# Performance work log

Hardware: AMD Instinct MI355X
Metric: run time of the kernel (lower is better)

Reference implementation:

```python
import jax, jax.numpy as jnp
import numpy as np

B, S, D = 4, 2048, 1024
EPS = 1e-5


def setup_inputs() -> dict:
    key = jax.random.key(0)
    ks = jax.random.split(key, 8)
    s = 1.0 / np.sqrt(D)
    return {
        "x": jax.random.normal(ks[0], (B, S, D), dtype=jnp.float32),
        "Wq": jax.random.normal(ks[1], (D, D), dtype=jnp.float32) * s,
        "Wk": jax.random.normal(ks[2], (D, D), dtype=jnp.float32) * s,
        "Wv": jax.random.normal(ks[3], (D, D), dtype=jnp.float32) * s,
        "W1": jax.random.normal(ks[4], (D, D), dtype=jnp.float32) * s,
        "b1": jnp.zeros((D,), dtype=jnp.float32),
        "W2": jax.random.normal(ks[5], (D, D), dtype=jnp.float32) * s,
        "b2": jnp.zeros((D,), dtype=jnp.float32),
        "gamma": jnp.ones((D,), dtype=jnp.float32),
        "beta": jnp.zeros((D,), dtype=jnp.float32),
    }


def _layer_norm(x, gamma, beta):
    mu = jnp.mean(x, axis=-1, keepdims=True)
    var = jnp.mean(jnp.square(x - mu), axis=-1, keepdims=True)
    return (x - mu) * jax.lax.rsqrt(var + EPS) * gamma + beta


def reference(x, Wq, Wk, Wv, W1, b1, W2, b2, gamma, beta):
    seq_len, d = x.shape[1], x.shape[2]
    # torch Linear: y = x @ W.T
    Q = jnp.einsum('bsd,ed->bse', x, Wq)
    K = jnp.einsum('bsd,ed->bse', x, Wk)
    V = jnp.einsum('bsd,ed,->bse', x, Wv, jnp.float32(1.0)) if False else jnp.einsum('bsd,ed->bse', x, Wv)
    scores = jnp.einsum('bqd,bkd->bqk', Q, K) / jnp.sqrt(jnp.float32(d))
    causal = jnp.tril(jnp.ones((seq_len, seq_len), dtype=bool))  # [S,S]
    scores = jnp.where(causal[None, :, :], scores, -jnp.inf)
    attn = jax.nn.softmax(scores, axis=-1)
    attn_out = jnp.einsum('bqk,bkd->bqd', attn, V)
    # dropout is identity at eval
    h = _layer_norm(x + attn_out, gamma, beta)
    ff = jnp.einsum('bsd,ed->bse', jax.nn.relu(jnp.einsum('bsd,ed->bse', h, W1) + b1), W2) + b2
    out = _layer_norm(h + ff, gamma, beta)
    return out
```

## Files before the change

kernel.cpp:

```cpp
#include <hip/hip_runtime.h>
#include <math.h>
#include <cstdint>
#include <cstddef>

#define DI __device__ __forceinline__

typedef __bf16 bf16x8 __attribute__((ext_vector_type(8)));
typedef float f32x4 __attribute__((ext_vector_type(4)));

static constexpr int kB = 4, kS = 2048, kD = 1024;
static constexpr int kM = kB * kS;
static constexpr float kScale = 0.03125f;
static constexpr float kEps = 1e-5f;

DI unsigned short f2bf(float f) {
  unsigned u = __float_as_uint(f);
  u += 0x7FFFu + ((u >> 16) & 1u);
  return (unsigned short)(u >> 16);
}
DI float bf2f(unsigned short h) {
  return __uint_as_float(((unsigned)h) << 16);
}

DI void gld_lds16(const void* g, void* l) {
  __builtin_amdgcn_global_load_lds(
      (__attribute__((address_space(1))) void*)(void*)g,
      (__attribute__((address_space(3))) void*)l, 16, 0, 0);
}

__global__ __launch_bounds__(256) void k_cast_all(
    const float* __restrict__ x, const float* __restrict__ Wq,
    const float* __restrict__ Wk, const float* __restrict__ Wv,
    const float* __restrict__ W1, const float* __restrict__ W2,
    unsigned short* __restrict__ xb, unsigned short* __restrict__ Wqkb,
    unsigned short* __restrict__ Wvb, unsigned short* __restrict__ W1b,
    unsigned short* __restrict__ W2b) {
  const int i = blockIdx.x * 256 + threadIdx.x;
  const int X4 = kM * kD / 4;
  const int W4 = kD * kD / 4;
  const float* src;
  unsigned short* dst;
  int j;
  if (i < X4) { src = x; dst = xb; j = i; }
  else if (i < X4 + W4)     { src = Wq; dst = Wqkb;          j = i - X4; }
  else if (i < X4 + 2 * W4) { src = Wk; dst = Wqkb + 4 * W4; j = i - X4 - W4; }
  else if (i < X4 + 3 * W4) { src = Wv; dst = Wvb;           j = i - X4 - 2 * W4; }
  else if (i < X4 + 4 * W4) { src = W1; dst = W1b;           j = i - X4 - 3 * W4; }
  else                      { src = W2; dst = W2b;           j = i - X4 - 4 * W4; }
  float4 v = ((const float4*)src)[j];
  ushort4 o;
  o.x = f2bf(v.x); o.y = f2bf(v.y); o.z = f2bf(v.z); o.w = f2bf(v.w);
  ((ushort4*)dst)[j] = o;
}

template <int OUT_BF16, int RELU, int CAUSAL>
__global__ __launch_bounds__(256, 2) void k_gemm_nt(
    const unsigned short* __restrict__ A, const unsigned short* __restrict__ B,
    void* __restrict__ Cv, const float* __restrict__ bias,
    int M, int N, int K, int lda, int ldb, int ldc,
    long sA, long sB, long sC) {
  int bm, bn;
  {
    int lin = blockIdx.x + gridDim.x * blockIdx.y;
    const int nblk = gridDim.x * gridDim.y;
    if ((nblk & 7) == 0)
      lin = (lin & 7) * (nblk >> 3) + (lin >> 3);
    if (CAUSAL == 1) {
      const int t = lin;
      int r = (int)floorf((sqrtf(8.f * (float)t + 1.f) - 1.f) * 0.5f);
      while ((r + 1) * (r + 2) / 2 <= t) ++r;
      while (r * (r + 1) / 2 > t) --r;
      bm = r * 128;
      bn = (t - r * (r + 1) / 2) * 128;
    } else {
      bm = (lin / gridDim.x) * 128;
      bn = (lin % gridDim.x) * 128;
    }
  }
  A += (long)blockIdx.z * sA;
  B += (long)blockIdx.z * sB;

  const int tid = threadIdx.x;
  const int lane = tid & 63;
  const int wm = ((tid >> 6) >> 1) * 64;
  const int wn = ((tid >> 6) & 1) * 64;

  __shared__ __align__(16) unsigned short Asm[128 * 64];
  __shared__ __align__(16) unsigned short Bsm[128 * 64];

  f32x4 acc[4][4];
#pragma unroll
  for (int i = 0; i < 4; ++i)
#pragma unroll
    for (int j = 0; j < 4; ++j) acc[i][j] = (f32x4){0.f, 0.f, 0.f, 0.f};

  const int r_row = tid >> 3;
  const int dst_k = (tid & 7) * 8;
  const int src_k = ((tid & 7) ^ ((tid >> 3) & 7)) * 8;
  const int fm = lane & 15;
  const int fq = lane >> 4;

  for (int k0 = 0; k0 < K; k0 += 64) {
#pragma unroll
    for (int i = 0; i < 4; ++i) {
      const int row = i * 32 + r_row;
      gld_lds16(A + (long)(bm + row) * lda + (k0 + src_k), Asm + row * 64 + dst_k);
      gld_lds16(B + (long)(bn + row) * ldb + (k0 + src_k), Bsm + row * 64 + dst_k);
    }
    __syncthreads();
#pragma unroll
    for (int kk = 0; kk < 2; ++kk) {
      bf16x8 af[4], bfr[4];
#pragma unroll
      for (int i = 0; i < 4; ++i) {
        const int pa = ((kk * 4 + fq) ^ (fm & 7)) * 8;
        af[i]  = *(const bf16x8*)(Asm + (wm + i * 16 + fm) * 64 + pa);
        bfr[i] = *(const bf16x8*)(Bsm + (wn + i * 16 + fm) * 64 + pa);
      }
#pragma unroll
      for (int i = 0; i < 4; ++i)
#pragma unroll
        for (int j = 0; j < 4; ++j)
          acc[i][j] = __builtin_amdgcn_mfma_f32_16x16x32_bf16(af[i], bfr[j], acc[i][j], 0, 0, 0);
    }
    __syncthreads();
  }

  const long cb = (long)blockIdx.z * sC;
#pragma unroll
  for (int i = 0; i < 4; ++i) {
#pragma unroll
    for (int j = 0; j < 4; ++j) {
      const int col = bn + wn + j * 16 + fm;
      const float bv = bias ? bias[col] : 0.f;
#pragma unroll
      for (int r = 0; r < 4; ++r) {
        const int row = bm + wm + i * 16 + fq * 4 + r;
        float v = acc[i][j][r] + bv;
        if (RELU) v = fmaxf(v, 0.f);
        if (OUT_BF16)
          ((unsigned short*)Cv)[cb + (long)row * ldc + col] = f2bf(v);
        else
          ((float*)Cv)[cb + (long)row * ldc + col] = v;
      }
    }
  }
}

__global__ __launch_bounds__(256, 2) void k_attn_pv(
    const unsigned short* __restrict__ P, const unsigned short* __restrict__ Vt,
    unsigned short* __restrict__ O) {
  const int r = blockIdx.x;
  const int q = blockIdx.y + 16 * blockIdx.z;
  const int lx = q & 7;
  const int pq = r + 8 * (q >> 3);
  const int pair = pq & 15;
  const int zz = pq >> 4;

  const int bn = lx * 128;
  const int bm_hi = (31 - pair) * 64;
  const int bm_lo = pair * 64;
  const int Khi = bm_hi + 64;
  const int Klo = bm_lo + 64;
  P  += (long)zz * kS * kS;
  Vt += (long)zz * kD * kS;
  O  += (long)zz * kS * kD;

  const int tid = threadIdx.x;
  const int lane = tid & 63;
  const int wn = (tid >> 6) * 32;

  __shared__ __align__(16) unsigned short Ah[64 * 64];
  __shared__ __align__(16) unsigned short Al[64 * 64];
  __shared__ __align__(16) unsigned short Bs[128 * 64];

  f32x4 ah[4][2], al[4][2];
#pragma unroll
  for (int i = 0; i < 4; ++i)
#pragma unroll
    for (int j = 0; j < 2; ++j) {
      ah[i][j] = (f32x4){0.f, 0.f, 0.f, 0.f};
      al[i][j] = (f32x4){0.f, 0.f, 0.f, 0.f};
    }

  const int r_row = tid >> 3;
  const int dst_k = (tid & 7) * 8;
  const int src_k = ((tid & 7) ^ ((tid >> 3) & 7)) * 8;
  const int fm = lane & 15;
  const int fq = lane >> 4;

  for (int k0 = 0; k0 < Khi; k0 += 64) {
    const bool lo = (k0 < Klo);
#pragma unroll
    for (int i = 0; i < 2; ++i) {
      const int row = i * 32 + r_row;
      gld_lds16(P + (long)(bm_hi + row) * kS + (k0 + src_k), Ah + row * 64 + dst_k);
      if (lo)
        gld_lds16(P + (long)(bm_lo + row) * kS + (k0 + src_k), Al + row * 64 + dst_k);
    }
#pragma unroll
    for (int i = 0; i < 4; ++i) {
      const int row = i * 32 + r_row;
      gld_lds16(Vt + (long)(bn + row) * kS + (k0 + src_k), Bs + row * 64 + dst_k);
    }
    __syncthreads();
#pragma unroll
    for (int kk = 0; kk < 2; ++kk) {
      bf16x8 afh[4], afl[4], bfr[2];
#pragma unroll
      for (int i = 0; i < 4; ++i) {
        const int ra = i * 16 + fm;
        const int pa = ((kk * 4 + fq) ^ (ra & 7)) * 8;
        afh[i] = *(const bf16x8*)(Ah + ra * 64 + pa);
        afl[i] = *(const bf16x8*)(Al + ra * 64 + pa);
      }
#pragma unroll
      for (int j = 0; j < 2; ++j) {
        const int rb = wn + j * 16 + fm;
        const int pb = ((kk * 4 + fq) ^ (rb & 7)) * 8;
        bfr[j] = *(const bf16x8*)(Bs + rb * 64 + pb);
      }
#pragma unroll
      for (int i = 0; i < 4; ++i)
#pragma unroll
        for (int j = 0; j < 2; ++j)
          ah[i][j] = __builtin_amdgcn_mfma_f32_16x16x32_bf16(afh[i], bfr[j], ah[i][j], 0, 0, 0);
      if (lo) {
#pragma unroll
        for (int i = 0; i < 4; ++i)
#pragma unroll
          for (int j = 0; j < 2; ++j)
            al[i][j] = __builtin_amdgcn_mfma_f32_16x16x32_bf16(afl[i], bfr[j], al[i][j], 0, 0, 0);
      }
    }
    __syncthreads();
  }

#pragma unroll
  for (int i = 0; i < 4; ++i) {
#pragma unroll
    for (int j = 0; j < 2; ++j) {
      const int col = bn + wn + j * 16 + fm;
#pragma unroll
      for (int r2 = 0; r2 < 4; ++r2) {
        const int rr = i * 16 + fq * 4 + r2;
        O[(long)(bm_hi + rr) * kD + col] = f2bf(ah[i][j][r2]);
        O[(long)(bm_lo + rr) * kD + col] = f2bf(al[i][j][r2]);
      }
    }
  }
}

DI float wsum(float v) {
  v += __shfl_xor(v, 32, 64);
  v += __shfl_xor(v, 16, 64);
  v += __shfl_xor(v, 8, 64);
  v += __shfl_xor(v, 4, 64);
  v += __shfl_xor(v, 2, 64);
  v += __shfl_xor(v, 1, 64);
  return v;
}
DI float wmax(float v) {
  v = fmaxf(v, __shfl_xor(v, 32, 64));
  v = fmaxf(v, __shfl_xor(v, 16, 64));
  v = fmaxf(v, __shfl_xor(v, 8, 64));
  v = fmaxf(v, __shfl_xor(v, 4, 64));
  v = fmaxf(v, __shfl_xor(v, 2, 64));
  v = fmaxf(v, __shfl_xor(v, 1, 64));
  return v;
}

__global__ __launch_bounds__(256) void k_softmax_causal(
    const unsigned short* __restrict__ S, unsigned short* __restrict__ P) {
  const int row = blockIdx.x;
  const int q = row & (kS - 1);
  const int lim = (q & ~127) + 128;
  const unsigned short* Srow = S + (long)row * kS;
  unsigned short* Prow = P + (long)row * kS;
  const int tid = threadIdx.x;
  __shared__ float red[4];

  float v[8];
  float mx = -INFINITY;
#pragma unroll
  for (int i = 0; i < 8; ++i) {
    const int k = tid + i * 256;
    float xv = -INFINITY;
    if (k <= q) xv = bf2f(Srow[k]) * kScale;
    v[i] = xv;
    mx = fmaxf(mx, xv);
  }
  mx = wmax(mx);
  if ((tid & 63) == 0) red[tid >> 6] = mx;
  __syncthreads();
  mx = fmaxf(fmaxf(red[0], red[1]), fmaxf(red[2], red[3]));
  __syncthreads();

  float sum = 0.f;
#pragma unroll
  for (int i = 0; i < 8; ++i) {
    const float e = (v[i] > -INFINITY) ? __expf(v[i] - mx) : 0.f;
    v[i] = e;
    sum += e;
  }
  sum = wsum(sum);
  if ((tid & 63) == 0) red[tid >> 6] = sum;
  __syncthreads();
  sum = red[0] + red[1] + red[2] + red[3];
  const float inv = 1.f / sum;
#pragma unroll
  for (int i = 0; i < 8; ++i) {
    const int k = tid + i * 256;
    if (k < lim) Prow[k] = f2bf(v[i] * inv);
  }
}

template <int X_BF16, int OUT_FP32>
__global__ __launch_bounds__(256) void k_residual_ln(
    const void* __restrict__ Xv, const unsigned short* __restrict__ Yb,
    const float* __restrict__ gamma, const float* __restrict__ beta,
    float* __restrict__ Out, unsigned short* __restrict__ OutB) {
  const long base = (long)blockIdx.x * kD;
  const int tid = threadIdx.x;
  __shared__ float reds[4], redss[4];
  float v[4];
  float s = 0.f, ss2 = 0.f;
#pragma unroll
  for (int i = 0; i < 4; ++i) {
    const int k = tid + i * 256;
    const float xf = X_BF16 ? bf2f(((const unsigned short*)Xv)[base + k])
                            : ((const float*)Xv)[base + k];
    const float xv = xf + bf2f(Yb[base + k]);
    v[i] = xv;
    s += xv;
    ss2 += xv * xv;
  }
  s = wsum(s);
  ss2 = wsum(ss2);
  if ((tid & 63) == 0) { reds[tid >> 6] = s; redss[tid >> 6] = ss2; }
  __syncthreads();
  s = reds[0] + reds[1] + reds[2] + reds[3];
  ss2 = redss[0] + redss[1] + redss[2] + redss[3];
  const float mu = s * (1.f / kD);
  float var = ss2 * (1.f / kD) - mu * mu;
  var = fmaxf(var, 0.f);
  const float rstd = rsqrtf(var + kEps);
#pragma unroll
  for (int i = 0; i < 4; ++i) {
    const int k = tid + i * 256;
    const float y = (v[i] - mu) * rstd * gamma[k] + beta[k];
    if (OUT_FP32) Out[base + k] = y;
    else          OutB[base + k] = f2bf(y);
  }
}

extern "C" void kernel_launch(void* const* d_in, const int* in_sizes, int n_in,
                              void* d_out, int out_size, void* d_ws, size_t ws_size,
                              hipStream_t stream) {
  (void)in_sizes; (void)n_in; (void)out_size; (void)ws_size;
  const float* x     = (const float*)d_in[0];
  const float* Wq    = (const float*)d_in[1];
  const float* Wk    = (const float*)d_in[2];
  const float* Wv    = (const float*)d_in[3];
  const float* W1    = (const float*)d_in[4];
  const float* b1    = (const float*)d_in[5];
  const float* W2    = (const float*)d_in[6];
  const float* b2    = (const float*)d_in[7];
  const float* gamma = (const float*)d_in[8];
  const float* beta  = (const float*)d_in[9];
  float* out = (float*)d_out;

  char* base = (char*)d_ws;
  size_t off = 0;
  auto alloc = [&](size_t bytes) -> void* {
    void* p = base + off;
    off = (off + bytes + 255) & ~(size_t)255;
    return p;
  };

  unsigned short* xb     = (unsigned short*)alloc((size_t)kM * kD * 2);
  unsigned short* Wqkb   = (unsigned short*)alloc((size_t)2 * kD * kD * 2);
  unsigned short* Wvb    = (unsigned short*)alloc((size_t)kD * kD * 2);
  unsigned short* W1b    = (unsigned short*)alloc((size_t)kD * kD * 2);
  unsigned short* W2b    = (unsigned short*)alloc((size_t)kD * kD * 2);
  unsigned short* QKb    = (unsigned short*)alloc((size_t)kM * 2 * kD * 2);
  unsigned short* Vt     = (unsigned short*)alloc((size_t)kM * kD * 2);
  unsigned short* Sb     = (unsigned short*)alloc((size_t)kB * kS * kS * 2);
  unsigned short* Pb     = (unsigned short*)alloc((size_t)kB * kS * kS * 2);
  unsigned short* attn_b = (unsigned short*)alloc((size_t)kM * kD * 2);
  unsigned short* ff_b = attn_b;
  unsigned short* hb   = Sb;
  unsigned short* mid  = Pb;

  dim3 blk(256);

  {
    const int n4 = (kM * kD + 5 * kD * kD) / 4;
    k_cast_all<<<n4 / 256, blk, 0, stream>>>(x, Wq, Wk, Wv, W1, W2,
                                             xb, Wqkb, Wvb, W1b, W2b);
  }

  k_gemm_nt<1, 0, 0><<<dim3(2 * kD / 128, kM / 128, 1), blk, 0, stream>>>(
      xb, Wqkb, QKb, nullptr, kM, 2 * kD, kD, kD, kD, 2 * kD, 0, 0, 0);

  k_gemm_nt<1, 0, 0><<<dim3(kS / 128, kD / 128, kB), blk, 0, stream>>>(
      Wvb, xb, Vt, nullptr, kD, kS, kD, kD, kD, kS,
      0, (long)kS * kD, (long)kD * kS);

  k_gemm_nt<1, 0, 1><<<dim3(136, 1, kB), blk, 0, stream>>>(
      QKb, QKb + kD, Sb, nullptr, kS, kS, kD, 2 * kD, 2 * kD, kS,
      (long)kS * 2 * kD, (long)kS * 2 * kD, (long)kS * kS);

  k_softmax_causal<<<kM, blk, 0, stream>>>(Sb, Pb);

  k_attn_pv<<<dim3(8, 16, kB), blk, 0, stream>>>(Pb, Vt, attn_b);

  k_residual_ln<0, 0><<<kM, blk, 0, stream>>>(x, attn_b, gamma, beta,
                                              nullptr, hb);

  k_gemm_nt<1, 1, 0><<<dim3(kD / 128, kM / 128, 1), blk, 0, stream>>>(
      hb, W1b, mid, b1, kM, kD, kD, kD, kD, kD, 0, 0, 0);
  k_gemm_nt<1, 0, 0><<<dim3(kD / 128, kM / 128, 1), blk, 0, stream>>>(
      mid, W2b, ff_b, b2, kM, kD, kD, kD, kD, kD, 0, 0, 0);

  k_residual_ln<1, 1><<<kM, blk, 0, stream>>>(hb, ff_b, gamma, beta,
                                              out, nullptr);
}
```

Baseline: 337.1 us.

## Add 8-wave 256-row GEMM with ping-pong LDS pipeline for projections and FFN

After: 329.5 us. 1.02x faster.

```diff
diff --git a/kernel.cpp b/kernel.cpp
--- a/kernel.cpp
+++ b/kernel.cpp
@@ -27,6 +27,9 @@
       (__attribute__((address_space(1))) void*)(void*)g,
       (__attribute__((address_space(3))) void*)l, 16, 0, 0);
 }
+
+#define SBAR() __builtin_amdgcn_sched_barrier(0)
+#define FULLBAR() do { SBAR(); __builtin_amdgcn_s_barrier(); SBAR(); } while (0)
 
 __global__ __launch_bounds__(256) void k_cast_all(
     const float* __restrict__ x, const float* __restrict__ Wq,
@@ -53,6 +56,181 @@
   ((ushort4*)dst)[j] = o;
 }
 
+template <int NF, int OUT_BF16, int RELU>
+__global__ __launch_bounds__(512, 2) void k_gemm8p(
+    const unsigned short* __restrict__ A, const unsigned short* __restrict__ B,
+    void* __restrict__ Cv, const float* __restrict__ bias,
+    int M, int N, int K, int lda, int ldb, int ldc,
+    long sA, long sB, long sC) {
+  constexpr int BN = NF * 64;
+  constexpr int LB = BN / 128;
+  constexpr int VM = 2 + 2 * LB;
+  constexpr int AH = 256 * 32;
+  constexpr int BH = BN * 32;
+
+  int lin = blockIdx.x + gridDim.x * blockIdx.y;
+  const int nblk = gridDim.x * gridDim.y;
+  if ((nblk & 7) == 0)
+    lin = (lin & 7) * (nblk >> 3) + (lin >> 3);
+  const int bm = (lin / gridDim.x) * 256;
+  const int bn = (lin % gridDim.x) * BN;
+  A += (long)blockIdx.z * sA;
+  B += (long)blockIdx.z * sB;
+
+  const int tid = threadIdx.x;
+  const int lane = tid & 63;
+  const int wm = (tid >> 6) >> 2;
+  const int wn = (tid >> 6) & 3;
+  const int fm = lane & 15;
+  const int fq = lane >> 4;
+
+  __shared__ __align__(16) unsigned short Asm[2 * 2 * AH];
+  __shared__ __align__(16) unsigned short Bsm[2 * 2 * BH];
+
+  long aoff[2];
+#pragma unroll
+  for (int i = 0; i < 2; ++i) {
+    const int ci = i * 512 + tid;
+    const int row = ci >> 2;
+    const int g = (ci & 3) ^ ((row >> 1) & 3);
+    aoff[i] = (long)(bm + row) * lda + g * 8;
+  }
+  long boff[LB];
+#pragma unroll
+  for (int i = 0; i < LB; ++i) {
+    const int ci = i * 512 + tid;
+    const int row = ci >> 2;
+    const int g = (ci & 3) ^ ((row >> 1) & 3);
+    boff[i] = (long)(bn + row) * ldb + g * 8;
+  }
+
+  const int NT = K >> 6;
+
+  auto stA = [&](int d, int kh, int t) {
+    const unsigned short* s = A + t * 64 + kh * 32;
+    unsigned short* dst = Asm + (d * 2 + kh) * AH;
+#pragma unroll
+    for (int i = 0; i < 2; ++i)
+      gld_lds16(s + aoff[i], dst + (i * 512 + tid) * 8);
+  };
+  auto stB = [&](int d, int kh, int t) {
+    const unsigned short* s = B + t * 64 + kh * 32;
+    unsigned short* dst = Bsm + (d * 2 + kh) * BH;
+#pragma unroll
+    for (int i = 0; i < LB; ++i)
+      gld_lds16(s + boff[i], dst + (i * 512 + tid) * 8);
+  };
+
+  const int slotoff = (fq ^ ((fm >> 1) & 3)) * 8;
+  const unsigned short* aRd = Asm + (wm * 128 + fm) * 32 + slotoff;
+  const unsigned short* bRd = Bsm + (wn * (NF * 16) + fm) * 32 + slotoff;
+
+  f32x4 acc[8][NF];
+#pragma unroll
+  for (int m = 0; m < 8; ++m)
+#pragma unroll
+    for (int n = 0; n < NF; ++n) acc[m][n] = (f32x4){0.f, 0.f, 0.f, 0.f};
+
+  stB(0, 0, 0); stA(0, 0, 0); stB(0, 1, 0); stA(0, 1, 0);
+  if (NT > 1) { stB(1, 0, 1); stA(1, 0, 1); stB(1, 1, 1); }
+  SBAR();
+  asm volatile("s_waitcnt vmcnt(%0)" :: "i"(VM) : "memory");
+  __builtin_amdgcn_s_barrier();
+  SBAR();
+
+  bf16x8 af[4], bfr[NF];
+
+  for (int t = 0; t < NT; ++t) {
+    const int d = t & 1;
+    const unsigned short* aB0 = aRd + d * (2 * AH);
+    const unsigned short* bB0 = bRd + d * (2 * BH);
+    const unsigned short* aB1 = aB0 + AH;
+    const unsigned short* bB1 = bB0 + BH;
+
+#pragma unroll
+    for (int m = 0; m < 4; ++m) af[m] = *(const bf16x8*)(aB0 + m * 512);
+#pragma unroll
+    for (int n = 0; n < NF; ++n) bfr[n] = *(const bf16x8*)(bB0 + n * 512);
+    if (t + 1 < NT) stA(d ^ 1, 1, t + 1);
+    FULLBAR();
+    __builtin_amdgcn_s_setprio(1);
+#pragma unroll
+    for (int m = 0; m < 4; ++m)
+#pragma unroll
+      for (int n = 0; n < NF; ++n)
+        acc[m][n] = __builtin_amdgcn_mfma_f32_16x16x32_bf16(af[m], bfr[n], acc[m][n], 0, 0, 0);
+    __builtin_amdgcn_s_setprio(0);
+    FULLBAR();
+
+#pragma unroll
+    for (int m = 0; m < 4; ++m) af[m] = *(const bf16x8*)(aB0 + (4 + m) * 512);
+    if (t + 2 < NT) stB(d, 0, t + 2);
+    FULLBAR();
+    __builtin_amdgcn_s_setprio(1);
+#pragma unroll
+    for (int m = 0; m < 4; ++m)
+#pragma unroll
+      for (int n = 0; n < NF; ++n)
+        acc[4 + m][n] = __builtin_amdgcn_mfma_f32_16x16x32_bf16(af[m], bfr[n], acc[4 + m][n], 0, 0, 0);
+    __builtin_amdgcn_s_setprio(0);
+    FULLBAR();
+
+#pragma unroll
+    for (int m = 0; m < 4; ++m) af[m] = *(const bf16x8*)(aB1 + m * 512);
+#pragma unroll
+    for (int n = 0; n < NF; ++n) bfr[n] = *(const bf16x8*)(bB1 + n * 512);
+    if (t + 2 < NT) stA(d, 0, t + 2);
+    FULLBAR();
+    __builtin_amdgcn_s_setprio(1);
+#pragma unroll
+    for (int m = 0; m < 4; ++m)
+#pragma unroll
+      for (int n = 0; n < NF; ++n)
+        acc[m][n] = __builtin_amdgcn_mfma_f32_16x16x32_bf16(af[m], bfr[n], acc[m][n], 0, 0, 0);
+    __builtin_amdgcn_s_setprio(0);
+    FULLBAR();
+
+#pragma unroll
+    for (int m = 0; m < 4; ++m) af[m] = *(const bf16x8*)(aB1 + (4 + m) * 512);
+    if (t + 2 < NT) stB(d, 1, t + 2);
+    SBAR();
+    if (t < NT - 2)
+      asm volatile("s_waitcnt vmcnt(%0)" :: "i"(VM) : "memory");
+    else
+      asm volatile("s_waitcnt vmcnt(0)" ::: "memory");
+    __builtin_amdgcn_s_barrier();
+    SBAR();
+    __builtin_amdgcn_s_setprio(1);
+#pragma unroll
+    for (int m = 0; m < 4; ++m)
+#pragma unroll
+      for (int n = 0; n < NF; ++n)
+        acc[4 + m][n] = __builtin_amdgcn_mfma_f32_16x16x32_bf16(af[m], bfr[n], acc[4 + m][n], 0, 0, 0);
+    __builtin_amdgcn_s_setprio(0);
+    FULLBAR();
+  }
+
+  const long cb = (long)blockIdx.z * sC;
+#pragma unroll
+  for (int n = 0; n < NF; ++n) {
+    const int col = bn + wn * (NF * 16) + n * 16 + fm;
+    const float bv = bias ? bias[col] : 0.f;
+#pragma unroll
+    for (int m = 0; m < 8; ++m) {
+#pragma unroll
+      for (int r = 0; r < 4; ++r) {
+        const int row = bm + wm * 128 + m * 16 + fq * 4 + r;
+        float v = acc[m][n][r] + bv;
+        if (RELU) v = fmaxf(v, 0.f);
+        if (OUT_BF16)
+          ((unsigned short*)Cv)[cb + (long)row * ldc + col] = f2bf(v);
+        else
+          ((float*)Cv)[cb + (long)row * ldc + col] = v;
+      }
+    }
+  }
+}
+
 template <int OUT_BF16, int RELU, int CAUSAL>
 __global__ __launch_bounds__(256, 2) void k_gemm_nt(
     const unsigned short* __restrict__ A, const unsigned short* __restrict__ B,
@@ -393,6 +571,7 @@
   unsigned short* mid  = Pb;
 
   dim3 blk(256);
+  dim3 blk8(512);
 
   {
     const int n4 = (kM * kD + 5 * kD * kD) / 4;
@@ -400,10 +579,10 @@
                                              xb, Wqkb, Wvb, W1b, W2b);
   }
 
-  k_gemm_nt<1, 0, 0><<<dim3(2 * kD / 128, kM / 128, 1), blk, 0, stream>>>(
+  k_gemm8p<4, 1, 0><<<dim3(2 * kD / 256, kM / 256, 1), blk8, 0, stream>>>(
       xb, Wqkb, QKb, nullptr, kM, 2 * kD, kD, kD, kD, 2 * kD, 0, 0, 0);
 
-  k_gemm_nt<1, 0, 0><<<dim3(kS / 128, kD / 128, kB), blk, 0, stream>>>(
+  k_gemm8p<2, 1, 0><<<dim3(kS / 128, kD / 256, kB), blk8, 0, stream>>>(
       Wvb, xb, Vt, nullptr, kD, kS, kD, kD, kD, kS,
       0, (long)kS * kD, (long)kD * kS);
 
@@ -418,9 +597,9 @@
   k_residual_ln<0, 0><<<kM, blk, 0, stream>>>(x, attn_b, gamma, beta,
                                               nullptr, hb);
 
-  k_gemm_nt<1, 1, 0><<<dim3(kD / 128, kM / 128, 1), blk, 0, stream>>>(
+  k_gemm8p<2, 1, 1><<<dim3(kD / 128, kM / 256, 1), blk8, 0, stream>>>(
       hb, W1b, mid, b1, kM, kD, kD, kD, kD, kD, 0, 0, 0);
-  k_gemm_nt<1, 0, 0><<<dim3(kD / 128, kM / 128, 1), blk, 0, stream>>>(
+  k_gemm8p<2, 1, 0><<<dim3(kD / 128, kM / 256, 1), blk8, 0, stream>>>(
       mid, W2b, ff_b, b2, kM, kD, kD, kD, kD, kD, 0, 0, 0);
 
   k_residual_ln<1, 1><<<kM, blk, 0, stream>>>(hb, ff_b, gamma, beta,
```
